# Kernel optimization log

Hardware: AMD Instinct MI355X
Metric: run time of the kernel (lower is better)

## Reference

```python
import jax, jax.numpy as jnp
import numpy as np

T, B, N_IN, H, N_OUT = 32, 32, 64, 256, 64
CLAMP_MIN, CLAMP_MAX = -2.0, 2.0  # scalar `min`/`max` forward args of the torch module


def setup_inputs() -> dict:
    key = jax.random.key(0)
    ks = jax.random.split(key, 8)
    s_ih = 1.0 / np.sqrt(N_IN)
    s_hh = 1.0 / np.sqrt(H)
    X = jax.random.normal(ks[0], (T, B, N_IN), jnp.float32)
    eps = jax.random.uniform(ks[1], (B,), jnp.float32) * 0.1  # per-sample perturbation radius
    W_ih = jax.random.normal(ks[2], (N_IN, H), jnp.float32) * s_ih  # already transposed, as in forward
    W_hh = jax.random.normal(ks[3], (H, H), jnp.float32) * s_hh
    b_ih = jax.random.normal(ks[4], (H,), jnp.float32) * s_hh
    b_hh = jax.random.normal(ks[5], (H,), jnp.float32) * s_hh
    W_o = jax.random.normal(ks[6], (H, N_OUT), jnp.float32) * s_hh
    b_o = jax.random.normal(ks[7], (N_OUT,), jnp.float32) * s_hh
    return dict(X=X, eps=eps, W_ih=W_ih, W_hh=W_hh, b_ih=b_ih, b_hh=b_hh, W_o=W_o, b_o=b_o)


def _zono_tanh(head, err):
    # DeepZ-style abstract tanh transformer on a zonotope (head [B,H], err [B,E,H]).
    rad = jnp.sum(jnp.abs(err), axis=1)                  # [B,H] concretization radius
    l, u = head - rad, head + rad
    tl, tu = jnp.tanh(l), jnp.tanh(u)
    lam = jnp.minimum(1.0 - tl * tl, 1.0 - tu * tu)      # minimal slope on [l,u]
    mu = 0.5 * (tu + tl - lam * (u + l))
    delta = 0.5 * (tu - tl - lam * (u - l))              # new error magnitude (>=0)
    new_head = lam * head + mu
    new_err = jnp.concatenate([lam[:, None, :] * err,
                               jax.vmap(jnp.diag)(delta)], axis=1)  # append H fresh symbols
    return new_head, new_err


def reference(X, eps, W_ih, W_hh, b_ih, b_hh, W_o, b_o):
    Bsz, Hn = X.shape[1], W_hh.shape[0]
    head_h = jnp.zeros((Bsz, Hn), X.dtype)
    err_h = jnp.zeros((Bsz, 0, Hn), X.dtype)
    bias = b_ih + b_hh
    for t in range(X.shape[0]):  # sequential recurrence; T is static
        x = X[t]                                          # [B, N_IN]
        l = jnp.maximum(x - eps[:, None], CLAMP_MIN)      # clamp(x-eps, min=min)
        u = jnp.minimum(x + eps[:, None], CLAMP_MAX)      # clamp(x+eps, max=max)
        head_x = 0.5 * (l + u)
        err_x = jax.vmap(jnp.diag)(0.5 * (u - l))         # diag_embed -> [B, N_IN, N_IN]
        # affine zonotope step: hx + hi + b_ih + b_hh
        head = head_x @ W_ih + head_h @ W_hh + bias       # [B, H]
        err = jnp.concatenate([err_h @ W_hh, err_x @ W_ih], axis=1)  # [B, E+N_IN, H]
        head_h, err_h = _zono_tanh(head, err)
    # output layer on the final zonotope; return concretized [lower, upper] bounds
    head_out = head_h @ W_o + b_o                         # [B, N_OUT]
    rad_out = jnp.sum(jnp.abs(err_h @ W_o), axis=1)       # [B, N_OUT]
    return jnp.stack([head_out - rad_out, head_out + rad_out])  # [2, B, N_OUT]
```

## Files before the change

kernel.cpp:

```cpp
#include <hip/hip_runtime.h>
#include <math.h>

typedef unsigned short u16;
typedef unsigned long long u64;
typedef __attribute__((ext_vector_type(8))) short bf16x8;
typedef __attribute__((ext_vector_type(4))) float f32x4;

#define T_STEPS 32
#define BSZ     32
#define N_IN    64
#define H       256
#define N_OUT   64
#define ESTRIDE 9984
#define CLAMP_MIN (-2.0f)
#define CLAMP_MAX ( 2.0f)
#define GNB 16


__device__ inline u16 f2bf(float x) {
    unsigned u = __builtin_bit_cast(unsigned, x);
    unsigned r = u + 0x7FFFu + ((u >> 16) & 1u);
    return (u16)(r >> 16);
}
__device__ inline float bf2f(short s) {
    return __builtin_bit_cast(float, ((unsigned)(u16)s) << 16);
}

__device__ __forceinline__ void gl_lds16(const u16* g, u16* l) {
    __builtin_amdgcn_global_load_lds(
        (const __attribute__((address_space(1))) unsigned int*)g,
        (__attribute__((address_space(3))) unsigned int*)l,
        16, 0, 0);
}

__device__ __forceinline__ float aload(const float* p) {
    return __hip_atomic_load(p, __ATOMIC_RELAXED, __HIP_MEMORY_SCOPE_AGENT);
}

__global__ void initarr_k(unsigned* arr) {
    arr[threadIdx.x + blockIdx.x * 256] = 0u;
}

__global__ void transpose_k(const float* __restrict__ src, float* __restrict__ dst,
                            int R, int C)
{
    __shared__ float tile[32][33];
    int bi = blockIdx.y, bj = blockIdx.x;
    int r0 = threadIdx.x >> 5, c = threadIdx.x & 31;
    #pragma unroll
    for (int rr = 0; rr < 4; ++rr) {
        int r = r0 * 4 + rr;
        tile[r][c] = src[(bi * 32 + r) * C + bj * 32 + c];
    }
    __syncthreads();
    #pragma unroll
    for (int rr = 0; rr < 4; ++rr) {
        int r = r0 * 4 + rr;
        dst[(bj * 32 + r) * R + bi * 32 + c] = tile[c][r];
    }
}

__global__ void packPairs_k(const float* __restrict__ W, float* __restrict__ WP)
{
    int p = blockIdx.x * 256 + threadIdx.x;
    int vb = (p & 1) * 2, hh = (p >> 1) & 1, m = (p >> 2) & 15, qq = (p >> 6) & 3;
    int KC = (p >> 8) & 7, RT = p >> 11;
    int i = RT * 16 + m, k = KC * 32 + qq * 8 + hh * 4 + vb;
    ((float2*)WP)[p] = make_float2(W[(size_t)i * H + k], W[(size_t)i * H + k + 1]);
}

__global__ void packWT_k(const float* __restrict__ WT32, u16* __restrict__ WTp)
{
    int p = blockIdx.x * 256 + threadIdx.x;
    int vb = (p & 1) * 2, hh = (p >> 1) & 1, m = (p >> 2) & 15, qq = (p >> 6) & 3;
    int KC = (p >> 8) & 7, RT = p >> 11;
    int n = RT * 16 + m, k = KC * 32 + qq * 8 + hh * 4 + vb;
    *(unsigned*)&WTp[2 * p] =
          (unsigned)f2bf(WT32[(size_t)n * H + k])
        | ((unsigned)f2bf(WT32[(size_t)n * H + k + 1]) << 16);
}

__global__ __launch_bounds__(256) void prefresh_k(
    const float* __restrict__ X, const float* __restrict__ eps,
    const float* __restrict__ Wih, const float* __restrict__ WihP,
    const float* __restrict__ bih, const float* __restrict__ bhh,
    u16* __restrict__ err, float* __restrict__ radT, float* __restrict__ hpX)
{
    __shared__ float rho_s[N_IN], hx_s[N_IN];
    const int t = blockIdx.x, bi = blockIdx.y, tid = threadIdx.x;
    if (tid < N_IN) {
        float x = X[((size_t)t * BSZ + bi) * N_IN + tid], e = eps[bi];
        float lo = fmaxf(x - e, CLAMP_MIN), up = fminf(x + e, CLAMP_MAX);
        rho_s[tid] = 0.5f * (up - lo);
        hx_s[tid]  = 0.5f * (up + lo);
    }
    __syncthreads();

    float s = 0.f, acc = bih[tid] + bhh[tid];
    #pragma unroll 8
    for (int i = 0; i < N_IN; ++i) {
        float w = Wih[(size_t)i * H + tid];
        s   += fabsf(rho_s[i]) * fabsf(w);
        acc += hx_s[i] * w;
    }
    radT[(size_t)t * BSZ * H + (size_t)bi * H + tid] = s;
    hpX [(size_t)t * BSZ * H + (size_t)bi * H + tid] = acc;

    u16* dst = err + (size_t)bi * ESTRIDE * H + (size_t)(20 * t) * 4096;
    const float2* wp = (const float2*)WihP;
    #pragma unroll 4
    for (int iter = 0; iter < 32; ++iter) {
        int p = iter * 256 + tid;
        int i = (p >> 11) * 16 + ((p >> 2) & 15);
        float2 w = wp[p];
        float rho = rho_s[i];
        *(unsigned*)&dst[2 * p] =
            (unsigned)f2bf(rho * w.x) | ((unsigned)f2bf(rho * w.y) << 16);
    }
}

__global__ __launch_bounds__(256, 2) void loop_k(
    const float* __restrict__ Whh, const float* __restrict__ WhhP,
    const u16* __restrict__ WhhTp,
    float* __restrict__ hpX, float* __restrict__ radT,
    u16* __restrict__ err, unsigned* __restrict__ arrive, int b0)
{
    __shared__ u16 sbuf[4][8192];
    __shared__ float lam_s[H], de_s[H], hh_s[H];
    const int bx = blockIdx.x, b = blockIdx.y, tid = threadIdx.x;
    const int babs = b0 + b;
    u16* errB = err + (size_t)b * ESTRIDE * H;
    const int wave = tid >> 6, lane = tid & 63;
    const int m = lane & 15, q = lane >> 4;

    #pragma unroll 1
    for (int t = 1; t < T_STEPS; ++t) {
        const int E_old = t * (N_IN + H);
        const int ntiles = (E_old - H) >> 5;
        const float* hpp  = hpX  + (size_t)(t - 1) * BSZ * H + (size_t)babs * H;
        float*       hpn  = hpX  + (size_t)t       * BSZ * H + (size_t)babs * H;
        const float* radp = radT + (size_t)(t - 1) * BSZ * H + (size_t)babs * H;
        float*       radn = radT + (size_t)t       * BSZ * H + (size_t)babs * H;
        const bool gem = (bx < ntiles);

        if (gem) {
            #pragma unroll
            for (int j = 0; j < 3; ++j) {
                int tj = bx + j * GNB;
                if (tj < ntiles) {
                    const u16* g = errB + (size_t)tj * 8192;
                    #pragma unroll
                    for (int r = 0; r < 4; ++r)
                        gl_lds16(g + r * 2048 + tid * 8,
                                 &sbuf[j][r * 2048 + wave * 512]);
                }
            }
        }
        bf16x8 bf[4][8];
        if (gem) {
            #pragma unroll
            for (int nt = 0; nt < 4; ++nt)
                #pragma unroll
                for (int kc = 0; kc < 8; ++kc)
                    bf[nt][kc] = *(const bf16x8*)
                        &WhhTp[(size_t)(((((wave * 4 + nt) * 8 + kc) * 4 + q) << 7) + m * 8)];
        }

        if (t > 1) {
            if (tid == 0) {
                const unsigned* a = &arrive[(t - 1) * BSZ + babs];
                while (__hip_atomic_load(a, __ATOMIC_RELAXED,
                                         __HIP_MEMORY_SCOPE_AGENT) < (unsigned)GNB)
                    __builtin_amdgcn_s_sleep(2);
            }
            __builtin_amdgcn_s_barrier();
        }

        {
            float hd = aload(&hpp[tid]), rv = aload(&radp[tid]);
            float lo = hd - rv, up = hd + rv;
            float tl = tanhf(lo), tu = tanhf(up);
            float la = fminf(1.f - tl * tl, 1.f - tu * tu);
            float mu = 0.5f * (tu + tl - la * (up + lo));
            float dd = 0.5f * (tu - tl - la * (up - lo));
            lam_s[tid] = la;
            de_s[tid]  = dd;
            hh_s[tid]  = la * hd + mu;
        }
        asm volatile("s_waitcnt lgkmcnt(0)" ::: "memory");
        __builtin_amdgcn_s_barrier();

        {
            const int dtile0 = 10 * t - 8;
            const float2* wp = (const float2*)WhhP;
            #pragma unroll
            for (int i = 0; i < 8; ++i) {
                int dt = dtile0 + i;
                if ((dt & 15) == bx) {
                    #pragma unroll
                    for (int rt2 = 0; rt2 < 2; ++rt2) {
                        int RTw = i * 2 + rt2;
                        u16* dst2 = errB + (size_t)(dt * 2 + rt2) * 4096;
                        const float2* wp2 = wp + (size_t)RTw * 2048;
                        #pragma unroll
                        for (int iter = 0; iter < 8; ++iter) {
                            int p = iter * 256 + tid;
                            int mm = (p >> 2) & 15;
                            float dv = de_s[RTw * 16 + mm];
                            float2 w = wp2[p];
                            *(unsigned*)&dst2[2 * p] =
                                (unsigned)f2bf(dv * w.x) | ((unsigned)f2bf(dv * w.y) << 16);
                        }
                    }
                }
            }
            float ss = 0.f, hacc = 0.f;
            #pragma unroll
            for (int ii = 0; ii < 16; ++ii) {
                int i = bx * 16 + ii;
                float w = Whh[(size_t)i * H + tid];
                ss   += fabsf(de_s[i]) * fabsf(w);
                hacc += hh_s[i] * w;
            }
            atomicAdd(&radn[tid], ss);
            atomicAdd(&hpn[tid], hacc);
        }

        if (gem) {
            #pragma unroll
            for (int nt = 0; nt < 4; ++nt)
                #pragma unroll
                for (int kc = 0; kc < 8; ++kc) {
                    const int k0 = kc * 32 + q * 8;
                    float4 la = *(const float4*)&lam_s[k0];
                    float4 lb = *(const float4*)&lam_s[k0 + 4];
                    bf16x8 w = bf[nt][kc], f;
                    f[0] = (short)f2bf(bf2f(w[0]) * la.x);
                    f[1] = (short)f2bf(bf2f(w[1]) * la.y);
                    f[2] = (short)f2bf(bf2f(w[2]) * la.z);
                    f[3] = (short)f2bf(bf2f(w[3]) * la.w);
                    f[4] = (short)f2bf(bf2f(w[4]) * lb.x);
                    f[5] = (short)f2bf(bf2f(w[5]) * lb.y);
                    f[6] = (short)f2bf(bf2f(w[6]) * lb.z);
                    f[7] = (short)f2bf(bf2f(w[7]) * lb.w);
                    bf[nt][kc] = f;
                }

            float racc[16];
            #pragma unroll
            for (int i = 0; i < 16; ++i) racc[i] = 0.f;

            asm volatile("s_waitcnt vmcnt(0)" ::: "memory");
            __builtin_amdgcn_s_barrier();

            int cur = 0;
            for (int tile = bx; tile < ntiles; tile += GNB) {
                int pf = tile + 3 * GNB;
                if (pf < ntiles) {
                    const u16* g = errB + (size_t)pf * 8192;
                    #pragma unroll
                    for (int r = 0; r < 4; ++r)
                        gl_lds16(g + r * 2048 + tid * 8,
                                 &sbuf[(cur + 3) & 3][r * 2048 + wave * 512]);
                }

                f32x4 acc[2][4];
                #pragma unroll
                for (int i = 0; i < 2; ++i)
                    #pragma unroll
                    for (int c = 0; c < 4; ++c) acc[i][c] = (f32x4){0.f, 0.f, 0.f, 0.f};

                #pragma unroll
                for (int kc = 0; kc < 8; ++kc) {
                    bf16x8 af[2];
                    #pragma unroll
                    for (int rt = 0; rt < 2; ++rt)
                        af[rt] = *(const bf16x8*)
                            &sbuf[cur][(((rt * 8 + kc) * 4 + q) << 7) + m * 8];
                    #pragma unroll
                    for (int nt = 0; nt < 4; ++nt)
                        #pragma unroll
                        for (int rt = 0; rt < 2; ++rt)
                            acc[rt][nt] = __builtin_amdgcn_mfma_f32_16x16x32_bf16(
                                bf[nt][kc], af[rt], acc[rt][nt], 0, 0, 0);
                }

                #pragma unroll
                for (int rt = 0; rt < 2; ++rt) {
                    const size_t rowbase = (size_t)(tile * 2 + rt) * 4096;
                    #pragma unroll
                    for (int nt = 0; nt < 4; ++nt) {
                        f32x4 v = acc[rt][nt];
                        racc[nt * 4 + 0] += fabsf(v[0]);
                        racc[nt * 4 + 1] += fabsf(v[1]);
                        racc[nt * 4 + 2] += fabsf(v[2]);
                        racc[nt * 4 + 3] += fabsf(v[3]);
                        unsigned lo = (unsigned)f2bf(v[0]) | ((unsigned)f2bf(v[1]) << 16);
                        unsigned hi = (unsigned)f2bf(v[2]) | ((unsigned)f2bf(v[3]) << 16);
                        const int NT  = wave * 4 + nt;
                        const int kcs = NT >> 1;
                        const int qq  = (NT & 1) * 2 + (q >> 1);
                        const size_t off16 = rowbase
                            + (size_t)(((kcs * 4 + qq) << 7) + m * 8 + (q & 1) * 4);
                        *(u64*)&errB[off16] = ((u64)hi << 32) | lo;
                    }
                }
                asm volatile("s_waitcnt vmcnt(32)" ::: "memory");
                __builtin_amdgcn_s_barrier();
                cur = (cur + 1) & 3;
            }

            #pragma unroll
            for (int i = 0; i < 16; ++i) {
                float v = racc[i];
                v += __shfl_xor(v, 1);
                v += __shfl_xor(v, 2);
                v += __shfl_xor(v, 4);
                v += __shfl_xor(v, 8);
                if (m == 0) {
                    int nt = i >> 2, vv = i & 3;
                    atomicAdd(&radn[wave * 64 + nt * 16 + q * 4 + vv], v);
                }
            }
        }

        asm volatile("s_waitcnt vmcnt(0)" ::: "memory");
        __syncthreads();
        if (tid == 0)
            __hip_atomic_fetch_add(&arrive[t * BSZ + babs], 1u,
                                   __ATOMIC_RELAXED, __HIP_MEMORY_SCOPE_AGENT);
    }
}

__global__ __launch_bounds__(256) void tanh_final_k(
    const float* __restrict__ hp, const float* __restrict__ rad,
    float* __restrict__ lam, float* __restrict__ de, float* __restrict__ head_h)
{
    const int b = blockIdx.x, h = threadIdx.x;
    float hd = hp[b * H + h], r = rad[b * H + h];
    float l = hd - r, u = hd + r;
    float tl = tanhf(l), tu = tanhf(u);
    float la = fminf(1.f - tl * tl, 1.f - tu * tu);
    float mu = 0.5f * (tu + tl - la * (u + l));
    float dd = 0.5f * (tu - tl - la * (u - l));
    lam[b * H + h] = la;
    de[b * H + h]  = dd;
    head_h[b * H + h] = la * hd + mu;
}

__global__ __launch_bounds__(256) void packWoT_k(
    const float* __restrict__ WoT32, const float* __restrict__ lam,
    u16* __restrict__ WoTp)
{
    const int b = blockIdx.x, tid = threadIdx.x;
    __shared__ float lam_s[H];
    lam_s[tid] = lam[b * H + tid];
    __syncthreads();
    u16* dst = WoTp + (size_t)b * N_OUT * H;
    #pragma unroll 4
    for (int iter = 0; iter < 32; ++iter) {
        int p = iter * 256 + tid;
        int vb = (p & 1) * 2, hh = (p >> 1) & 1, m = (p >> 2) & 15, qq = (p >> 6) & 3;
        int KC = (p >> 8) & 7, RT = p >> 11;
        int n = RT * 16 + m, k = KC * 32 + qq * 8 + hh * 4 + vb;
        *(unsigned*)&dst[2 * p] =
              (unsigned)f2bf(lam_s[k]     * WoT32[(size_t)n * H + k])
            | ((unsigned)f2bf(lam_s[k + 1] * WoT32[(size_t)n * H + k + 1]) << 16);
    }
}

__global__ void head_out_k(
    const float* __restrict__ head_h, const float* __restrict__ de,
    const float* __restrict__ Wo, const float* __restrict__ bo,
    float* __restrict__ head_out, float* __restrict__ rad_out)
{
    const int b = blockIdx.x, o = threadIdx.x;
    float acc = bo[o], accR = 0.f;
    #pragma unroll 4
    for (int j = 0; j < H; ++j) {
        float w = Wo[j * N_OUT + o];
        acc  += head_h[b * H + j] * w;
        accR += fabsf(de[b * H + j] * w);
    }
    head_out[b * N_OUT + o] = acc;
    rad_out[b * N_OUT + o]  = accR;
}

__global__ __launch_bounds__(256) void gemm_out_k(
    const u16* __restrict__ err, const u16* __restrict__ WoTp,
    float* __restrict__ rad_out)
{
    __shared__ float rad_s[N_OUT];
    const int b = blockIdx.y, row0 = blockIdx.x * 256, tid = threadIdx.x;
    const int wave = tid >> 6, lane = tid & 63;
    const int m = lane & 15, q = lane >> 4;
    const u16* errB = err + (size_t)b * ESTRIDE * H;
    const u16* Wb   = WoTp + (size_t)b * N_OUT * H;

    if (tid < N_OUT) rad_s[tid] = 0.f;
    __syncthreads();

    f32x4 acc[4][4];
    #pragma unroll
    for (int i = 0; i < 4; ++i)
        #pragma unroll
        for (int c = 0; c < 4; ++c) acc[i][c] = (f32x4){0.f, 0.f, 0.f, 0.f};

    const int tile0 = (row0 >> 4) + wave * 4;
    #pragma unroll
    for (int kc = 0; kc < 8; ++kc) {
        bf16x8 af[4], bw[4];
        #pragma unroll
        for (int rt = 0; rt < 4; ++rt)
            af[rt] = *(const bf16x8*)
                &errB[(size_t)(((((tile0 + rt) * 8 + kc) * 4 + q) << 7) + m * 8)];
        #pragma unroll
        for (int nt = 0; nt < 4; ++nt)
            bw[nt] = *(const bf16x8*)
                &Wb[(size_t)((((nt * 8 + kc) * 4 + q) << 7) + m * 8)];
        #pragma unroll
        for (int nt = 0; nt < 4; ++nt)
            #pragma unroll
            for (int rt = 0; rt < 4; ++rt)
                acc[rt][nt] = __builtin_amdgcn_mfma_f32_16x16x32_bf16(
                    af[rt], bw[nt], acc[rt][nt], 0, 0, 0);
    }
    #pragma unroll
    for (int nt = 0; nt < 4; ++nt) {
        float s = 0.f;
        #pragma unroll
        for (int rt = 0; rt < 4; ++rt)
            #pragma unroll
            for (int r = 0; r < 4; ++r) s += fabsf(acc[rt][nt][r]);
        atomicAdd(&rad_s[nt * 16 + m], s);
    }
    __syncthreads();
    if (tid < N_OUT) atomicAdd(&rad_out[b * N_OUT + tid], rad_s[tid]);
}

__global__ void combine_k(const float* __restrict__ head_out,
                          const float* __restrict__ rad_out,
                          float* __restrict__ out)
{
    int i = blockIdx.x * 256 + threadIdx.x;
    if (i < BSZ * N_OUT) {
        float h = head_out[i], r = rad_out[i];
        out[i]               = h - r;
        out[BSZ * N_OUT + i] = h + r;
    }
}

extern "C" void kernel_launch(void* const* d_in, const int* in_sizes, int n_in,
                              void* d_out, int out_size, void* d_ws, size_t ws_size,
                              hipStream_t stream)
{
    const float* X    = (const float*)d_in[0];
    const float* eps  = (const float*)d_in[1];
    const float* Wih  = (const float*)d_in[2];
    const float* Whh  = (const float*)d_in[3];
    const float* bih  = (const float*)d_in[4];
    const float* bhh  = (const float*)d_in[5];
    const float* Wo   = (const float*)d_in[6];
    const float* bo   = (const float*)d_in[7];
    float* out = (float*)d_out;

    const size_t per_sample = (size_t)ESTRIDE * H * 2 + (size_t)N_OUT * H * 2;
    const size_t shared_b = (size_t)H * H * 4
                          + (size_t)N_OUT * H * 4
                          + (size_t)N_IN * H * 4
                          + (size_t)H * H * 4
                          + (size_t)H * H * 2
                          + (size_t)T_STEPS * BSZ * H * 4
                          + (size_t)T_STEPS * BSZ * H * 4
                          + (size_t)3 * BSZ * H * 4
                          + (size_t)2 * BSZ * N_OUT * 4
                          + (size_t)T_STEPS * BSZ * 4 + 512;
    int Bc = BSZ;
    while (Bc > 1 && (size_t)Bc * per_sample + shared_b > ws_size) Bc >>= 1;

    char* p = (char*)d_ws;
    u16* errP      = (u16*)p;   p += (size_t)Bc * ESTRIDE * H * 2;
    u16* WoTp      = (u16*)p;   p += (size_t)Bc * N_OUT * H * 2;
    u16* WhhTp     = (u16*)p;   p += (size_t)H * H * 2;
    float* WhhT32  = (float*)p; p += (size_t)H * H * 4;
    float* WoT32   = (float*)p; p += (size_t)N_OUT * H * 4;
    float* WihP    = (float*)p; p += (size_t)N_IN * H * 4;
    float* WhhP    = (float*)p; p += (size_t)H * H * 4;
    float* hpX     = (float*)p; p += (size_t)T_STEPS * BSZ * H * 4;
    float* radT    = (float*)p; p += (size_t)T_STEPS * BSZ * H * 4;
    float* lam     = (float*)p; p += (size_t)BSZ * H * 4;
    float* de      = (float*)p; p += (size_t)BSZ * H * 4;
    float* head_h  = (float*)p; p += (size_t)BSZ * H * 4;
    float* head_out= (float*)p; p += (size_t)BSZ * N_OUT * 4;
    float* rad_out = (float*)p; p += (size_t)BSZ * N_OUT * 4 + 64;
    unsigned* arrive = (unsigned*)p;

    initarr_k<<<(T_STEPS * BSZ) / 256, 256, 0, stream>>>(arrive);
    transpose_k<<<dim3(H / 32, H / 32), 256, 0, stream>>>(Whh, WhhT32, H, H);
    transpose_k<<<dim3(N_OUT / 32, H / 32), 256, 0, stream>>>(Wo, WoT32, H, N_OUT);
    packPairs_k<<<(N_IN * 128) / 256, 256, 0, stream>>>(Wih, WihP);
    packPairs_k<<<(H * 128) / 256, 256, 0, stream>>>(Whh, WhhP);
    packWT_k<<<128, 256, 0, stream>>>(WhhT32, WhhTp);

    for (int b0 = 0; b0 < BSZ; b0 += Bc) {
        prefresh_k<<<dim3(T_STEPS, Bc), 256, 0, stream>>>(
            X + (size_t)b0 * N_IN, eps + b0, Wih, WihP, bih, bhh, errP,
            radT + (size_t)b0 * H, hpX + (size_t)b0 * H);

        loop_k<<<dim3(GNB, Bc), 256, 0, stream>>>(
            Whh, WhhP, WhhTp, hpX, radT, errP, arrive, b0);

        const float* hp_last  = hpX  + (size_t)(T_STEPS - 1) * BSZ * H + (size_t)b0 * H;
        const float* rad_last = radT + (size_t)(T_STEPS - 1) * BSZ * H + (size_t)b0 * H;
        tanh_final_k<<<Bc, 256, 0, stream>>>(
            hp_last, rad_last, lam + (size_t)b0 * H, de + (size_t)b0 * H,
            head_h + (size_t)b0 * H);
        packWoT_k<<<Bc, 256, 0, stream>>>(WoT32, lam + (size_t)b0 * H, WoTp);
        head_out_k<<<Bc, 64, 0, stream>>>(
            head_h + (size_t)b0 * H, de + (size_t)b0 * H, Wo, bo,
            head_out + (size_t)b0 * N_OUT, rad_out + (size_t)b0 * N_OUT);
        gemm_out_k<<<dim3(ESTRIDE / 256, Bc), 256, 0, stream>>>(
            errP, WoTp, rad_out + (size_t)b0 * N_OUT);
    }

    combine_k<<<(BSZ * N_OUT + 255) / 256, 256, 0, stream>>>(head_out, rad_out, out);
}
```

Baseline: 1.646 ms.

## Fuse final tanh and output-layer GEMM into persistent recurrence kernel

Moves the final tanh transformer, head/output projection and the error-times-W_o radius GEMM into the tail of the persistent loop kernel. Each block waits on the last-step arrival counter, builds the lam-scaled W_o fragments in registers from a shared pre-packed bf16 W_o, and streams its share of error tiles through a 4-deep LDS prefetch ring. This removes four kernel launches and the per-sample packed W_o buffer. In exchange it adds a spin-wait, atomic accumulation into head_out and rad_out (now zeroed up front), and a final GEMM spread over only 16 blocks per sample.

Result: slower. 1.723 ms (+4.7%).

```diff
diff --git a/kernel.cpp b/kernel.cpp
--- a/kernel.cpp
+++ b/kernel.cpp
@@ -37,8 +37,9 @@
     return __hip_atomic_load(p, __ATOMIC_RELAXED, __HIP_MEMORY_SCOPE_AGENT);
 }
 
-__global__ void initarr_k(unsigned* arr) {
-    arr[threadIdx.x + blockIdx.x * 256] = 0u;
+__global__ void zero_k(unsigned* ptr, int n) {
+    int i = blockIdx.x * 256 + threadIdx.x;
+    if (i < n) ptr[i] = 0u;
 }
 
 __global__ void transpose_k(const float* __restrict__ src, float* __restrict__ dst,
@@ -121,8 +122,10 @@
 
 __global__ __launch_bounds__(256, 2) void loop_k(
     const float* __restrict__ Whh, const float* __restrict__ WhhP,
-    const u16* __restrict__ WhhTp,
+    const u16* __restrict__ WhhTp, const u16* __restrict__ WoTps,
+    const float* __restrict__ Wo, const float* __restrict__ bo,
     float* __restrict__ hpX, float* __restrict__ radT,
+    float* __restrict__ head_out, float* __restrict__ rad_out,
     u16* __restrict__ err, unsigned* __restrict__ arrive, int b0)
 {
     __shared__ u16 sbuf[4][8192];
@@ -330,112 +333,130 @@
             __hip_atomic_fetch_add(&arrive[t * BSZ + babs], 1u,
                                    __ATOMIC_RELAXED, __HIP_MEMORY_SCOPE_AGENT);
     }
-}
-
-__global__ __launch_bounds__(256) void tanh_final_k(
-    const float* __restrict__ hp, const float* __restrict__ rad,
-    float* __restrict__ lam, float* __restrict__ de, float* __restrict__ head_h)
-{
-    const int b = blockIdx.x, h = threadIdx.x;
-    float hd = hp[b * H + h], r = rad[b * H + h];
-    float l = hd - r, u = hd + r;
-    float tl = tanhf(l), tu = tanhf(u);
-    float la = fminf(1.f - tl * tl, 1.f - tu * tu);
-    float mu = 0.5f * (tu + tl - la * (u + l));
-    float dd = 0.5f * (tu - tl - la * (u - l));
-    lam[b * H + h] = la;
-    de[b * H + h]  = dd;
-    head_h[b * H + h] = la * hd + mu;
-}
-
-__global__ __launch_bounds__(256) void packWoT_k(
-    const float* __restrict__ WoT32, const float* __restrict__ lam,
-    u16* __restrict__ WoTp)
-{
-    const int b = blockIdx.x, tid = threadIdx.x;
-    __shared__ float lam_s[H];
-    lam_s[tid] = lam[b * H + tid];
-    __syncthreads();
-    u16* dst = WoTp + (size_t)b * N_OUT * H;
-    #pragma unroll 4
-    for (int iter = 0; iter < 32; ++iter) {
-        int p = iter * 256 + tid;
-        int vb = (p & 1) * 2, hh = (p >> 1) & 1, m = (p >> 2) & 15, qq = (p >> 6) & 3;
-        int KC = (p >> 8) & 7, RT = p >> 11;
-        int n = RT * 16 + m, k = KC * 32 + qq * 8 + hh * 4 + vb;
-        *(unsigned*)&dst[2 * p] =
-              (unsigned)f2bf(lam_s[k]     * WoT32[(size_t)n * H + k])
-            | ((unsigned)f2bf(lam_s[k + 1] * WoT32[(size_t)n * H + k + 1]) << 16);
-    }
-}
-
-__global__ void head_out_k(
-    const float* __restrict__ head_h, const float* __restrict__ de,
-    const float* __restrict__ Wo, const float* __restrict__ bo,
-    float* __restrict__ head_out, float* __restrict__ rad_out)
-{
-    const int b = blockIdx.x, o = threadIdx.x;
-    float acc = bo[o], accR = 0.f;
-    #pragma unroll 4
-    for (int j = 0; j < H; ++j) {
-        float w = Wo[j * N_OUT + o];
-        acc  += head_h[b * H + j] * w;
-        accR += fabsf(de[b * H + j] * w);
-    }
-    head_out[b * N_OUT + o] = acc;
-    rad_out[b * N_OUT + o]  = accR;
-}
-
-__global__ __launch_bounds__(256) void gemm_out_k(
-    const u16* __restrict__ err, const u16* __restrict__ WoTp,
-    float* __restrict__ rad_out)
-{
-    __shared__ float rad_s[N_OUT];
-    const int b = blockIdx.y, row0 = blockIdx.x * 256, tid = threadIdx.x;
-    const int wave = tid >> 6, lane = tid & 63;
-    const int m = lane & 15, q = lane >> 4;
-    const u16* errB = err + (size_t)b * ESTRIDE * H;
-    const u16* Wb   = WoTp + (size_t)b * N_OUT * H;
-
-    if (tid < N_OUT) rad_s[tid] = 0.f;
-    __syncthreads();
-
-    f32x4 acc[4][4];
-    #pragma unroll
-    for (int i = 0; i < 4; ++i)
+
+    {
+        const int ntiles = 10 * T_STEPS - 8;
+        const float* hpp  = hpX  + (size_t)(T_STEPS - 1) * BSZ * H + (size_t)babs * H;
+        const float* radp = radT + (size_t)(T_STEPS - 1) * BSZ * H + (size_t)babs * H;
+
         #pragma unroll
-        for (int c = 0; c < 4; ++c) acc[i][c] = (f32x4){0.f, 0.f, 0.f, 0.f};
-
-    const int tile0 = (row0 >> 4) + wave * 4;
-    #pragma unroll
-    for (int kc = 0; kc < 8; ++kc) {
-        bf16x8 af[4], bw[4];
+        for (int j = 0; j < 3; ++j) {
+            const u16* g = errB + (size_t)(bx + j * GNB) * 8192;
+            #pragma unroll
+            for (int r = 0; r < 4; ++r)
+                gl_lds16(g + r * 2048 + tid * 8, &sbuf[j][r * 2048 + wave * 512]);
+        }
+        bf16x8 bw[8];
         #pragma unroll
-        for (int rt = 0; rt < 4; ++rt)
-            af[rt] = *(const bf16x8*)
-                &errB[(size_t)(((((tile0 + rt) * 8 + kc) * 4 + q) << 7) + m * 8)];
+        for (int kc = 0; kc < 8; ++kc)
+            bw[kc] = *(const bf16x8*)
+                &WoTps[(size_t)((((wave * 8 + kc) * 4 + q) << 7) + m * 8)];
+
+        if (tid == 0) {
+            const unsigned* a = &arrive[(T_STEPS - 1) * BSZ + babs];
+            while (__hip_atomic_load(a, __ATOMIC_RELAXED,
+                                     __HIP_MEMORY_SCOPE_AGENT) < (unsigned)GNB)
+                __builtin_amdgcn_s_sleep(2);
+        }
+        __builtin_amdgcn_s_barrier();
+
+        {
+            float hd = aload(&hpp[tid]), rv = aload(&radp[tid]);
+            float lo = hd - rv, up = hd + rv;
+            float tl = tanhf(lo), tu = tanhf(up);
+            float la = fminf(1.f - tl * tl, 1.f - tu * tu);
+            float mu = 0.5f * (tu + tl - la * (up + lo));
+            float dd = 0.5f * (tu - tl - la * (up - lo));
+            lam_s[tid] = la;
+            de_s[tid]  = dd;
+            hh_s[tid]  = la * hd + mu;
+        }
+        asm volatile("s_waitcnt lgkmcnt(0)" ::: "memory");
+        __builtin_amdgcn_s_barrier();
+
+        if (tid < N_OUT) {
+            float hacc = (bx == 0) ? bo[tid] : 0.f, ss = 0.f;
+            #pragma unroll
+            for (int ii = 0; ii < 16; ++ii) {
+                int j = bx * 16 + ii;
+                float w = Wo[(size_t)j * N_OUT + tid];
+                hacc += hh_s[j] * w;
+                ss   += fabsf(de_s[j] * w);
+            }
+            atomicAdd(&head_out[babs * N_OUT + tid], hacc);
+            atomicAdd(&rad_out [babs * N_OUT + tid], ss);
+        }
+
         #pragma unroll
-        for (int nt = 0; nt < 4; ++nt)
-            bw[nt] = *(const bf16x8*)
-                &Wb[(size_t)((((nt * 8 + kc) * 4 + q) << 7) + m * 8)];
+        for (int kc = 0; kc < 8; ++kc) {
+            const int k0 = kc * 32 + q * 8;
+            float4 la = *(const float4*)&lam_s[k0];
+            float4 lb = *(const float4*)&lam_s[k0 + 4];
+            bf16x8 w = bw[kc], f;
+            f[0] = (short)f2bf(bf2f(w[0]) * la.x);
+            f[1] = (short)f2bf(bf2f(w[1]) * la.y);
+            f[2] = (short)f2bf(bf2f(w[2]) * la.z);
+            f[3] = (short)f2bf(bf2f(w[3]) * la.w);
+            f[4] = (short)f2bf(bf2f(w[4]) * lb.x);
+            f[5] = (short)f2bf(bf2f(w[5]) * lb.y);
+            f[6] = (short)f2bf(bf2f(w[6]) * lb.z);
+            f[7] = (short)f2bf(bf2f(w[7]) * lb.w);
+            bw[kc] = f;
+        }
+
+        float racc[4] = {0.f, 0.f, 0.f, 0.f};
+        asm volatile("s_waitcnt vmcnt(0)" ::: "memory");
+        __builtin_amdgcn_s_barrier();
+
+        int cur = 0;
+        for (int tile = bx; tile < ntiles; tile += GNB) {
+            int pf = tile + 3 * GNB;
+            if (pf < ntiles) {
+                const u16* g = errB + (size_t)pf * 8192;
+                #pragma unroll
+                for (int r = 0; r < 4; ++r)
+                    gl_lds16(g + r * 2048 + tid * 8,
+                             &sbuf[(cur + 3) & 3][r * 2048 + wave * 512]);
+            }
+
+            f32x4 acc[2];
+            acc[0] = (f32x4){0.f, 0.f, 0.f, 0.f};
+            acc[1] = (f32x4){0.f, 0.f, 0.f, 0.f};
+            #pragma unroll
+            for (int kc = 0; kc < 8; ++kc) {
+                bf16x8 af[2];
+                #pragma unroll
+                for (int rt = 0; rt < 2; ++rt)
+                    af[rt] = *(const bf16x8*)
+                        &sbuf[cur][(((rt * 8 + kc) * 4 + q) << 7) + m * 8];
+                #pragma unroll
+                for (int rt = 0; rt < 2; ++rt)
+                    acc[rt] = __builtin_amdgcn_mfma_f32_16x16x32_bf16(
+                        bw[kc], af[rt], acc[rt], 0, 0, 0);
+            }
+            #pragma unroll
+            for (int rt = 0; rt < 2; ++rt) {
+                racc[0] += fabsf(acc[rt][0]);
+                racc[1] += fabsf(acc[rt][1]);
+                racc[2] += fabsf(acc[rt][2]);
+                racc[3] += fabsf(acc[rt][3]);
+            }
+            asm volatile("s_waitcnt vmcnt(8)" ::: "memory");
+            __builtin_amdgcn_s_barrier();
+            cur = (cur + 1) & 3;
+        }
+
         #pragma unroll
-        for (int nt = 0; nt < 4; ++nt)
-            #pragma unroll
-            for (int rt = 0; rt < 4; ++rt)
-                acc[rt][nt] = __builtin_amdgcn_mfma_f32_16x16x32_bf16(
-                    af[rt], bw[nt], acc[rt][nt], 0, 0, 0);
-    }
-    #pragma unroll
-    for (int nt = 0; nt < 4; ++nt) {
-        float s = 0.f;
-        #pragma unroll
-        for (int rt = 0; rt < 4; ++rt)
-            #pragma unroll
-            for (int r = 0; r < 4; ++r) s += fabsf(acc[rt][nt][r]);
-        atomicAdd(&rad_s[nt * 16 + m], s);
-    }
-    __syncthreads();
-    if (tid < N_OUT) atomicAdd(&rad_out[b * N_OUT + tid], rad_s[tid]);
+        for (int v = 0; v < 4; ++v) {
+            float s = racc[v];
+            s += __shfl_xor(s, 1);
+            s += __shfl_xor(s, 2);
+            s += __shfl_xor(s, 4);
+            s += __shfl_xor(s, 8);
+            if (m == 0)
+                atomicAdd(&rad_out[babs * N_OUT + wave * 16 + q * 4 + v], s);
+        }
+    }
 }
 
 __global__ void combine_k(const float* __restrict__ head_out,
@@ -464,43 +485,42 @@
     const float* bo   = (const float*)d_in[7];
     float* out = (float*)d_out;
 
-    const size_t per_sample = (size_t)ESTRIDE * H * 2 + (size_t)N_OUT * H * 2;
+    const size_t per_sample = (size_t)ESTRIDE * H * 2;
     const size_t shared_b = (size_t)H * H * 4
                           + (size_t)N_OUT * H * 4
                           + (size_t)N_IN * H * 4
                           + (size_t)H * H * 4
                           + (size_t)H * H * 2
+                          + (size_t)N_OUT * H * 2
                           + (size_t)T_STEPS * BSZ * H * 4
                           + (size_t)T_STEPS * BSZ * H * 4
-                          + (size_t)3 * BSZ * H * 4
                           + (size_t)2 * BSZ * N_OUT * 4
-                          + (size_t)T_STEPS * BSZ * 4 + 512;
+                          + (size_t)T_STEPS * BSZ * 4 + 1024;
     int Bc = BSZ;
     while (Bc > 1 && (size_t)Bc * per_sample + shared_b > ws_size) Bc >>= 1;
 
     char* p = (char*)d_ws;
     u16* errP      = (u16*)p;   p += (size_t)Bc * ESTRIDE * H * 2;
-    u16* WoTp      = (u16*)p;   p += (size_t)Bc * N_OUT * H * 2;
     u16* WhhTp     = (u16*)p;   p += (size_t)H * H * 2;
+    u16* WoTps     = (u16*)p;   p += (size_t)N_OUT * H * 2;
     float* WhhT32  = (float*)p; p += (size_t)H * H * 4;
     float* WoT32   = (float*)p; p += (size_t)N_OUT * H * 4;
     float* WihP    = (float*)p; p += (size_t)N_IN * H * 4;
     float* WhhP    = (float*)p; p += (size_t)H * H * 4;
     float* hpX     = (float*)p; p += (size_t)T_STEPS * BSZ * H * 4;
     float* radT    = (float*)p; p += (size_t)T_STEPS * BSZ * H * 4;
-    float* lam     = (float*)p; p += (size_t)BSZ * H * 4;
-    float* de      = (float*)p; p += (size_t)BSZ * H * 4;
-    float* head_h  = (float*)p; p += (size_t)BSZ * H * 4;
     float* head_out= (float*)p; p += (size_t)BSZ * N_OUT * 4;
-    float* rad_out = (float*)p; p += (size_t)BSZ * N_OUT * 4 + 64;
+    float* rad_out = (float*)p; p += (size_t)BSZ * N_OUT * 4;
     unsigned* arrive = (unsigned*)p;
-
-    initarr_k<<<(T_STEPS * BSZ) / 256, 256, 0, stream>>>(arrive);
+    const int nzero = 2 * BSZ * N_OUT + T_STEPS * BSZ;
+
+    zero_k<<<(nzero + 255) / 256, 256, 0, stream>>>((unsigned*)head_out, nzero);
     transpose_k<<<dim3(H / 32, H / 32), 256, 0, stream>>>(Whh, WhhT32, H, H);
     transpose_k<<<dim3(N_OUT / 32, H / 32), 256, 0, stream>>>(Wo, WoT32, H, N_OUT);
     packPairs_k<<<(N_IN * 128) / 256, 256, 0, stream>>>(Wih, WihP);
     packPairs_k<<<(H * 128) / 256, 256, 0, stream>>>(Whh, WhhP);
     packWT_k<<<128, 256, 0, stream>>>(WhhT32, WhhTp);
+    packWT_k<<<32, 256, 0, stream>>>(WoT32, WoTps);
 
     for (int b0 = 0; b0 < BSZ; b0 += Bc) {
         prefresh_k<<<dim3(T_STEPS, Bc), 256, 0, stream>>>(
@@ -508,19 +528,8 @@
             radT + (size_t)b0 * H, hpX + (size_t)b0 * H);
 
         loop_k<<<dim3(GNB, Bc), 256, 0, stream>>>(
-            Whh, WhhP, WhhTp, hpX, radT, errP, arrive, b0);
-
-        const float* hp_last  = hpX  + (size_t)(T_STEPS - 1) * BSZ * H + (size_t)b0 * H;
-        const float* rad_last = radT + (size_t)(T_STEPS - 1) * BSZ * H + (size_t)b0 * H;
-        tanh_final_k<<<Bc, 256, 0, stream>>>(
-            hp_last, rad_last, lam + (size_t)b0 * H, de + (size_t)b0 * H,
-            head_h + (size_t)b0 * H);
-        packWoT_k<<<Bc, 256, 0, stream>>>(WoT32, lam + (size_t)b0 * H, WoTp);
-        head_out_k<<<Bc, 64, 0, stream>>>(
-            head_h + (size_t)b0 * H, de + (size_t)b0 * H, Wo, bo,
-            head_out + (size_t)b0 * N_OUT, rad_out + (size_t)b0 * N_OUT);
-        gemm_out_k<<<dim3(ESTRIDE / 256, Bc), 256, 0, stream>>>(
-            errP, WoTp, rad_out + (size_t)b0 * N_OUT);
+            Whh, WhhP, WhhTp, WoTps, Wo, bo, hpX, radT,
+            head_out, rad_out, errP, arrive, b0);
     }
 
     combine_k<<<(BSZ * N_OUT + 255) / 256, 256, 0, stream>>>(head_out, rad_out, out);
```
